# Kernel tuning notes

Hardware: AMD Instinct MI355X
Metric: run time of the kernel (lower is better)

Reference implementation:

```python
import jax, jax.numpy as jnp
import numpy as np

KERNEL_SIZES = [2, 4, 8, 16, 32, 64]
MAXK = max(k + k // 2 for k in KERNEL_SIZES[1:])  # 96
PAD_LO = (MAXK - 1) // 2  # 47
PAD_HI = MAXK - 1 - PAD_LO  # 48


def _alternating(K, even_negative):
    f = np.ones(K, np.float32)
    idx = np.arange(K)
    mask = (idx % 2 == 0) if even_negative else (idx % 2 == 1)
    f[mask] = -1.0
    return f


def make_weight_bank():
    """Builds all 17 fixed filters, zero-padded and center-aligned into one
    (17, 1, MAXK) bank so a single 'same'-padded conv matches 17 torch convs.
    Alignment: torch pads left=(K-1)//2 for kernel K; embedding each kernel at
    offset (MAXK-1)//2 - (K-1)//2 inside a MAXK kernel padded (PAD_LO, PAD_HI)
    reproduces the identical output."""
    filters = []
    for K in KERNEL_SIZES:              # group 1: -1 at even indices
        filters.append(_alternating(K, True))
    for K in KERNEL_SIZES:              # group 2: -1 at odd indices
        filters.append(_alternating(K, False))
    for K in KERNEL_SIZES[1:]:          # group 3: piecewise quadratic, len K + K//2
        q = K // 4
        left = (np.linspace(0.0, 1.0, q + 1, dtype=np.float32)[1:]) ** 2
        right = left[::-1]
        filters.append(np.concatenate([-left, -right, 2 * left, 2 * right, -left, -right]).astype(np.float32))
    W = np.zeros((len(filters), 1, MAXK), np.float32)
    for i, f in enumerate(filters):
        K = len(f)
        o = (MAXK - 1) // 2 - (K - 1) // 2
        W[i, 0, o:o + K] = f
    return jnp.asarray(W)


def setup_inputs() -> dict:
    key = jax.random.key(0)
    x = jax.random.normal(key, (128, 1, 32768), dtype=jnp.float32)
    W = make_weight_bank()  # (17, 1, 96), fixed non-trainable filters
    return {"x": x, "W": W}


def reference(x, W):
    # x: (B, 1, L); W: (17, 1, MAXK). One cross-correlation conv = bank of 17
    # 'same'-padded conv1d filters; then ReLU.
    y = jax.lax.conv_general_dilated(
        x, W,
        window_strides=(1,),
        padding=[(PAD_LO, PAD_HI)],
        dimension_numbers=("NCH", "OIH", "NCH"),
    )
    return jax.nn.relu(y)  # (B, 17, L)
```

## Files before the change

### kernel.cpp

```cpp
#include <hip/hip_runtime.h>


#define S_LEN    32768
#define NFILT    17
#define TILE     1024
#define HALO_L   47
#define WIN      (TILE + 96)
#define NTHREADS 256
#define NCHUNKS  25

struct BankT {
    float w[11][96];
    constexpr BankT() : w{} {
        const int KS[6] = {2, 4, 8, 16, 32, 64};
        for (int fi = 0; fi < 6; ++fi) {
            const int K = KS[fi];
            const int o = 47 - (K - 1) / 2;
            for (int i = 0; i < K; ++i)
                w[fi][o + i] = (i % 2 == 0) ? -1.0f : 1.0f;
        }
        for (int fi = 0; fi < 5; ++fi) {
            const int K = KS[fi + 1];
            const int Q = K / 4;
            const int o = 47 - (3 * K / 2 - 1) / 2;
            for (int j = 0; j < 6 * Q; ++j) {
                const int seg = j / Q, i = j - seg * Q;
                const float t = (seg == 0 || seg == 2 || seg == 4)
                                ? (float)(i + 1) / (float)Q
                                : (float)(Q - i) / (float)Q;
                const float v = t * t;
                w[fi + 6][o + j] = (seg == 2 || seg == 3) ? 2.0f * v : -v;
            }
        }
    }
};
__constant__ constexpr BankT BANK;

__global__ __launch_bounds__(NTHREADS)
void conv_bank_kernel(const float* __restrict__ x, float* __restrict__ out) {
    __shared__ float xs[WIN];

    const int tid = threadIdx.x;
    const int ts  = blockIdx.x * TILE;
    const int b   = blockIdx.y;
    const float* __restrict__ xrow = x + (size_t)b * S_LEN;

#pragma unroll
    for (int j0 = 0; j0 < WIN; j0 += NTHREADS) {
        const int j = j0 + tid;
        if (j0 + NTHREADS <= WIN || j < WIN) {
            const int g = ts - HALO_L + j;
            xs[j] = ((unsigned)g < (unsigned)S_LEN) ? xrow[g] : 0.0f;
        }
    }
    __syncthreads();

    float acc[11][4];
#pragma unroll
    for (int f = 0; f < 11; ++f)
#pragma unroll
        for (int r = 0; r < 4; ++r) acc[f][r] = 0.0f;

    const float4* __restrict__ xv4 = reinterpret_cast<const float4*>(xs) + tid;
#pragma unroll
    for (int c = 0; c < NCHUNKS; ++c) {
        const float4 xq = xv4[c];
        const float xe[4] = {xq.x, xq.y, xq.z, xq.w};
#pragma unroll
        for (int l = 0; l < 4; ++l) {
            const int d = 4 * c + l;
#pragma unroll
            for (int r = 0; r < 4; ++r) {
                const int k = d - r;
                if (k >= 0 && k < 96) {
#pragma unroll
                    for (int f = 0; f < 11; ++f) {
                        const float wv = BANK.w[f][k];
                        if (wv != 0.0f)
                            acc[f][r] = fmaf(wv, xe[l], acc[f][r]);
                    }
                }
            }
        }
    }

    const int t0 = ts + 4 * tid;
    float* __restrict__ obase = out + (size_t)b * NFILT * S_LEN + t0;

    auto store_relu = [&](int row, float a0, float a1, float a2, float a3) {
        const float4 s = make_float4(fmaxf(a0, 0.f), fmaxf(a1, 0.f),
                                     fmaxf(a2, 0.f), fmaxf(a3, 0.f));
        *reinterpret_cast<float4*>(obase + (size_t)row * S_LEN) = s;
    };

#pragma unroll
    for (int f = 0; f < 6; ++f) {
        store_relu(f,      acc[f][0],  acc[f][1],  acc[f][2],  acc[f][3]);
        store_relu(f + 6, -acc[f][0], -acc[f][1], -acc[f][2], -acc[f][3]);
    }
#pragma unroll
    for (int f = 0; f < 5; ++f)
        store_relu(12 + f, acc[6 + f][0], acc[6 + f][1],
                           acc[6 + f][2], acc[6 + f][3]);
}

extern "C" void kernel_launch(void* const* d_in, const int* in_sizes, int n_in,
                              void* d_out, int out_size, void* d_ws, size_t ws_size,
                              hipStream_t stream) {
    const float* x = (const float*)d_in[0];
    float* out = (float*)d_out;
    const int nbatch = in_sizes[0] / S_LEN;
    dim3 grid(S_LEN / TILE, nbatch, 1);
    conv_bank_kernel<<<grid, NTHREADS, 0, stream>>>(x, out);
}
```

Measured before the change: 306.2 us.

## Compute alternating-sign filters via prefix sums and widen per-thread outputs to 8

Replaces the direct FMAs for the six alternating ±1 filters with a per-thread running alternating prefix sum, so each output becomes a difference of two prefix values. Per-thread outputs grow from 4 to 8, which amortises the shared-memory window reads over more outputs. An XOR-free padding swizzle is added to the shared-memory layout to reduce bank conflicts, and stores use nontemporal hints. The cost is higher register pressure from the 89-entry prefix array plus 40 accumulators, which may lower occupancy, and fewer blocks per row.

New measurement: 1.099 ms. 3.59x slower.

```diff
diff --git a/kernel.cpp b/kernel.cpp
--- a/kernel.cpp
+++ b/kernel.cpp
@@ -3,42 +3,43 @@
 
 #define S_LEN    32768
 #define NFILT    17
-#define TILE     1024
-#define HALO_L   47
+#define R        8
+#define NTHREADS 256
+#define TILE     (R * NTHREADS)
 #define WIN      (TILE + 96)
-#define NTHREADS 256
-#define NCHUNKS  25
+#define NCHUNK   26
+#define LDS_SZ   2416
 
-struct BankT {
-    float w[11][96];
-    constexpr BankT() : w{} {
-        const int KS[6] = {2, 4, 8, 16, 32, 64};
-        for (int fi = 0; fi < 6; ++fi) {
-            const int K = KS[fi];
-            const int o = 47 - (K - 1) / 2;
-            for (int i = 0; i < K; ++i)
-                w[fi][o + i] = (i % 2 == 0) ? -1.0f : 1.0f;
-        }
-        for (int fi = 0; fi < 5; ++fi) {
-            const int K = KS[fi + 1];
-            const int Q = K / 4;
+typedef float f32x4 __attribute__((ext_vector_type(4)));
+
+__host__ __device__ constexpr int swz(int j) { return j + 4 * (j >> 5); }
+
+__host__ __device__ constexpr bool neededT(int d) {
+    return (d >= 17 && d <= 24) || (d >= 33 && d <= 72) || (d >= 81 && d <= 88);
+}
+
+struct Bump {
+    float w[5][96];
+    constexpr Bump() : w{} {
+        const int KS[5] = {4, 8, 16, 32, 64};
+        for (int f = 0; f < 5; ++f) {
+            const int K = KS[f], Q = K / 4;
             const int o = 47 - (3 * K / 2 - 1) / 2;
             for (int j = 0; j < 6 * Q; ++j) {
                 const int seg = j / Q, i = j - seg * Q;
-                const float t = (seg == 0 || seg == 2 || seg == 4)
-                                ? (float)(i + 1) / (float)Q
-                                : (float)(Q - i) / (float)Q;
+                const float t = (seg % 2 == 0) ? (float)(i + 1) / (float)Q
+                                               : (float)(Q - i) / (float)Q;
                 const float v = t * t;
-                w[fi + 6][o + j] = (seg == 2 || seg == 3) ? 2.0f * v : -v;
+                w[f][o + j] = (seg == 2 || seg == 3) ? 2.0f * v : -v;
             }
         }
     }
 };
-__constant__ constexpr BankT BANK;
+__constant__ constexpr Bump BUMP;
 
 __global__ __launch_bounds__(NTHREADS)
 void conv_bank_kernel(const float* __restrict__ x, float* __restrict__ out) {
-    __shared__ float xs[WIN];
+    __shared__ float xs[LDS_SZ];
 
     const int tid = threadIdx.x;
     const int ts  = blockIdx.x * TILE;
@@ -49,59 +50,76 @@
     for (int j0 = 0; j0 < WIN; j0 += NTHREADS) {
         const int j = j0 + tid;
         if (j0 + NTHREADS <= WIN || j < WIN) {
-            const int g = ts - HALO_L + j;
-            xs[j] = ((unsigned)g < (unsigned)S_LEN) ? xrow[g] : 0.0f;
+            const int g = ts - 48 + j;
+            xs[swz(j)] = ((unsigned)g < (unsigned)S_LEN) ? xrow[g] : 0.0f;
         }
     }
     __syncthreads();
 
-    float acc[11][4];
+    float acc[5][R];
 #pragma unroll
-    for (int f = 0; f < 11; ++f)
+    for (int f = 0; f < 5; ++f)
 #pragma unroll
-        for (int r = 0; r < 4; ++r) acc[f][r] = 0.0f;
+        for (int r = 0; r < R; ++r) acc[f][r] = 0.0f;
 
-    const float4* __restrict__ xv4 = reinterpret_cast<const float4*>(xs) + tid;
+    float Tv[89];
+    float run = 0.0f;
+    const int base = R * tid;
+
 #pragma unroll
-    for (int c = 0; c < NCHUNKS; ++c) {
-        const float4 xq = xv4[c];
+    for (int c = 0; c < NCHUNK; ++c) {
+        const f32x4 xq = *reinterpret_cast<const f32x4*>(&xs[swz(base + 4 * c)]);
         const float xe[4] = {xq.x, xq.y, xq.z, xq.w};
 #pragma unroll
         for (int l = 0; l < 4; ++l) {
             const int d = 4 * c + l;
+            if (neededT(d)) Tv[d] = run;
+            if (d < 88) run += (d & 1) ? -xe[l] : xe[l];
 #pragma unroll
-            for (int r = 0; r < 4; ++r) {
-                const int k = d - r;
+            for (int r = 0; r < R; ++r) {
+                const int k = d - r - 1;
                 if (k >= 0 && k < 96) {
 #pragma unroll
-                    for (int f = 0; f < 11; ++f) {
-                        const float wv = BANK.w[f][k];
-                        if (wv != 0.0f)
-                            acc[f][r] = fmaf(wv, xe[l], acc[f][r]);
+                    for (int f = 0; f < 5; ++f) {
+                        const float wv = BUMP.w[f][k];
+                        if (wv != 0.0f) acc[f][r] = fmaf(wv, xe[l], acc[f][r]);
                     }
                 }
             }
         }
     }
 
-    const int t0 = ts + 4 * tid;
+    const int t0 = ts + base;
     float* __restrict__ obase = out + (size_t)b * NFILT * S_LEN + t0;
 
-    auto store_relu = [&](int row, float a0, float a1, float a2, float a3) {
-        const float4 s = make_float4(fmaxf(a0, 0.f), fmaxf(a1, 0.f),
-                                     fmaxf(a2, 0.f), fmaxf(a3, 0.f));
-        *reinterpret_cast<float4*>(obase + (size_t)row * S_LEN) = s;
+    auto st = [&](int row, const float (&v)[R]) {
+        float* p = obase + (size_t)row * S_LEN;
+        f32x4 lo, hi;
+        lo.x = fmaxf(v[0], 0.f); lo.y = fmaxf(v[1], 0.f);
+        lo.z = fmaxf(v[2], 0.f); lo.w = fmaxf(v[3], 0.f);
+        hi.x = fmaxf(v[4], 0.f); hi.y = fmaxf(v[5], 0.f);
+        hi.z = fmaxf(v[6], 0.f); hi.w = fmaxf(v[7], 0.f);
+        __builtin_nontemporal_store(lo, reinterpret_cast<f32x4*>(p));
+        __builtin_nontemporal_store(hi, reinterpret_cast<f32x4*>(p) + 1);
     };
 
+    const int KS[6] = {2, 4, 8, 16, 32, 64};
 #pragma unroll
-    for (int f = 0; f < 6; ++f) {
-        store_relu(f,      acc[f][0],  acc[f][1],  acc[f][2],  acc[f][3]);
-        store_relu(f + 6, -acc[f][0], -acc[f][1], -acc[f][2], -acc[f][3]);
+    for (int fi = 0; fi < 6; ++fi) {
+        const int K = KS[fi], h = (K - 1) / 2;
+        float a[R], n[R];
+#pragma unroll
+        for (int r = 0; r < R; ++r) {
+            const int dlo = r + 48 - h;
+            const float D = Tv[dlo + K] - Tv[dlo];
+            a[r] = (dlo & 1) ? D : -D;
+            n[r] = (dlo & 1) ? -D : D;
+        }
+        st(fi, a);
+        st(fi + 6, n);
     }
 #pragma unroll
-    for (int f = 0; f < 5; ++f)
-        store_relu(12 + f, acc[6 + f][0], acc[6 + f][1],
-                           acc[6 + f][2], acc[6 + f][3]);
+    for (int f = 0; f < 5; ++f) st(12 + f, acc[f]);
 }
 
 extern "C" void kernel_launch(void* const* d_in, const int* in_sizes, int n_in,
```
